# Kernel optimization log

Hardware: AMD Instinct MI355X
Metric: run time of the kernel (lower is better)

Reference implementation:

```python
import jax, jax.numpy as jnp
import numpy as np

NC = 6          # tessellation cells
THETA_D = 5     # null-space dim with zero boundary
NSTEPS = 100    # Euler integration steps for CPAB ODE
LN_EPS = 1e-5


def _cpab_basis():
    # per-cell affine params [a_i, b_i], i=0..5, vector len 12
    L = np.zeros((NC - 1 + 2, 2 * NC), dtype=np.float64)
    r = 0
    for j in range(1, NC):  # continuity at interior knots x_j = j/NC
        xj = j / NC
        L[r, 2 * (j - 1)] = xj; L[r, 2 * (j - 1) + 1] = 1.0
        L[r, 2 * j] = -xj;      L[r, 2 * j + 1] = -1.0
        r += 1
    L[r, 1] = 1.0; r += 1                                  # v(0)=0 -> b_0 = 0
    L[r, 2 * (NC - 1)] = 1.0; L[r, 2 * (NC - 1) + 1] = 1.0  # v(1)=0 -> a_5 + b_5 = 0
    _, S, Vt = np.linalg.svd(L)
    B = Vt[len(S):].T  # [12, 5] orthonormal null-space basis
    return jnp.asarray(B, dtype=jnp.float32)

B_BASIS = _cpab_basis()


def cpab_transform_grid(grid, theta):
    # grid [t] in [0,1]; theta [N, 5] -> transformed grid [N, t]
    N = theta.shape[0]
    A = (theta @ B_BASIS.T).reshape(N, NC, 2)  # [N, 6, 2] per-cell (a, b)
    x = jnp.broadcast_to(grid[None, :], (N, grid.shape[0]))
    h = 1.0 / NSTEPS

    def step(xc, _):
        idx = jnp.clip((xc * NC).astype(jnp.int32), 0, NC - 1)
        a = jnp.take_along_axis(A[:, :, 0], idx, axis=1)
        b = jnp.take_along_axis(A[:, :, 1], idx, axis=1)
        xn = jnp.clip(xc + h * (a * xc + b), 0.0, 1.0)
        return xn, None

    x, _ = jax.lax.scan(step, x, None, length=NSTEPS)
    return x


def interpolate1d(data, grid):
    # data [N, c, t]; grid [N, t_out] in [0,1] -> [N, c, t_out]
    t = data.shape[-1]
    pos = grid * (t - 1)
    x0 = jnp.clip(jnp.floor(pos).astype(jnp.int32), 0, t - 2)
    w = (pos - x0.astype(pos.dtype))[:, None, :]
    i0 = jnp.broadcast_to(x0[:, None, :], (data.shape[0], data.shape[1], grid.shape[1]))
    d0 = jnp.take_along_axis(data, i0, axis=2)
    d1 = jnp.take_along_axis(data, i0 + 1, axis=2)
    return d0 * (1.0 - w) + d1 * w


def transform_data(data, theta, t_out):
    grid = jnp.linspace(0.0, 1.0, t_out, dtype=data.dtype)
    return interpolate1d(data, cpab_transform_grid(grid, theta))


def images_to_pixels(x):
    # x [t,b,c,h,w] -> [b*h*w, c, t]
    t, b, c, h, w = x.shape
    return jnp.transpose(x, (1, 3, 4, 2, 0)).reshape(-1, c, t)


def layer_norm(x, w, b):
    m = x.mean(-1, keepdims=True)
    v = ((x - m) ** 2).mean(-1, keepdims=True)
    return (x - m) * jax.lax.rsqrt(v + LN_EPS) * w + b


def localise(x, ln_in_w, ln_in_b, conv1_w, conv1_b, conv2_w, conv2_b, ln_conv_w, ln_conv_b):
    # x [t,b,c,h,w] -> per-pixel features [b*h*w, F, t]
    t, b, c, h, w = x.shape
    z = jnp.transpose(x.reshape(t * b, c, h, w), (0, 2, 3, 1))  # [tb,h,w,c]
    z = layer_norm(z, ln_in_w, ln_in_b)
    z = jax.nn.relu(jnp.einsum('nhwc,cf->nhwf', z, conv1_w) + conv1_b)  # 1x1 conv
    z = jax.nn.relu(jnp.einsum('nhwf,fg->nhwg', z, conv2_w) + conv2_b)  # 1x1 conv
    z = layer_norm(z, ln_conv_w, ln_conv_b)
    F = z.shape[-1]
    z = z.reshape(t, b, h, w, F)
    return jnp.transpose(z, (1, 2, 3, 4, 0)).reshape(-1, F, t)


def setup_inputs() -> dict:
    key = jax.random.key(0)
    ks = jax.random.split(key, 6)
    t, b, c, h, w, F = 52, 4, 9, 64, 64, 64
    N = b * h * w
    din = 2 * F * t  # 6656
    return {
        'x': jax.random.normal(ks[0], (t, b, c, h, w), jnp.float32),
        'theta_shift_raw': jax.random.normal(ks[1], (N, THETA_D), jnp.float32),
        'ln_in_w': jnp.ones((c,), jnp.float32),
        'ln_in_b': jnp.zeros((c,), jnp.float32),
        'conv1_w': jax.random.normal(ks[2], (c, F), jnp.float32) / np.sqrt(c),
        'conv1_b': jnp.zeros((F,), jnp.float32),
        'conv2_w': jax.random.normal(ks[3], (F, F), jnp.float32) / np.sqrt(F),
        'conv2_b': jnp.zeros((F,), jnp.float32),
        'ln_conv_w': jnp.ones((F,), jnp.float32),
        'ln_conv_b': jnp.zeros((F,), jnp.float32),
        'fc1_w': jax.random.normal(ks[4], (din, 16), jnp.float32) / np.sqrt(din),
        'fc1_b': jnp.zeros((16,), jnp.float32),
        'fc2_w': jax.random.normal(ks[5], (16, THETA_D), jnp.float32) * 0.01,
        'fc2_b': jnp.zeros((THETA_D,), jnp.float32),
    }


def reference(x, theta_shift_raw, ln_in_w, ln_in_b, conv1_w, conv1_b, conv2_w, conv2_b,
              ln_conv_w, ln_conv_b, fc1_w, fc1_b, fc2_w, fc2_b):
    t, b, c, h, w = x.shape
    theta_scale = 0.5
    theta_shift = theta_scale * theta_shift_raw  # sampled transformation

    x_pix = images_to_pixels(x)  # [N, c, t]
    x_shift_pix = transform_data(x_pix, theta_shift, t)  # [N, c, t]
    # back to image stack [t,b,c,h,w]
    x_shift_img = jnp.transpose(x_shift_pix.reshape(b, h, w, c, t), (4, 0, 3, 1, 2))

    loc_args = (ln_in_w, ln_in_b, conv1_w, conv1_b, conv2_w, conv2_b, ln_conv_w, ln_conv_b)
    x_orig_loc = localise(x, *loc_args)           # [N, F, t]
    x_shift_loc = localise(x_shift_img, *loc_args)

    x_cat = jnp.concatenate((x_orig_loc, x_shift_loc), axis=1)  # [N, 2F, t]
    x_cat = x_cat.reshape(x_cat.shape[0], -1)                    # [N, 2F*t]
    theta_pred = jnp.tanh(jax.nn.relu(x_cat @ fc1_w + fc1_b) @ fc2_w + fc2_b)

    x_aligned = transform_data(x_pix, theta_pred, t)
    return (x_aligned, x_shift_pix, theta_pred, theta_shift)
```

## Files before the change

kernel.cpp:

```cpp
#include <hip/hip_runtime.h>
#include <math.h>

#define TT   52
#define BBAT 4
#define CCH  9
#define HWP  4096
#define FF   64
#define NP   16384
#define TD   5
#define NCC  6
#define TSTRIDE 147456

#define OUT0 0
#define OUT1 (NP*CCH*TT)
#define OUT2 (2*NP*CCH*TT)
#define OUT3 (OUT2 + NP*TD)

#define WS_BF    0
#define WS_WIMG  1024
#define WS_AIMG  4096
#define WS_XPIX  69632

typedef __attribute__((ext_vector_type(8)))  short short8v;
typedef __attribute__((ext_vector_type(4)))  float f32x4;
typedef __attribute__((ext_vector_type(4)))  int   int4v;
typedef __attribute__((ext_vector_type(2)))  int   int2v;

__device__ __forceinline__ unsigned bfb(float f) {
    unsigned x = __builtin_bit_cast(unsigned, f);
    return (x + 0x7fffu + ((x >> 16) & 1u)) >> 16;
}
__device__ __forceinline__ unsigned pk2(float a, float b) {
    return bfb(a) | (bfb(b) << 16);
}
__device__ __forceinline__ unsigned cvtpk(float a, float b) {
    unsigned r;
    asm("v_cvt_pk_bf16_f32 %0, %1, %2" : "=v"(r) : "v"(a), "v"(b));
    return r;
}
__device__ __forceinline__ int nswz(int n) {
    return (((n ^ (n >> 3)) & 1) << 6) | (((n >> 1) & 3) << 4);
}

__global__ __launch_bounds__(256) void k_pre(
    const float* __restrict__ lniw, const float* __restrict__ lnib,
    const float* __restrict__ w1c,  const float* __restrict__ b1c,
    const float* __restrict__ w2c,  const float* __restrict__ fc1w,
    const float* __restrict__ x,
    float* __restrict__ Bout, int4v* __restrict__ wimg,
    int4v* __restrict__ aimg, float* __restrict__ xp, int use_xp)
{
    __shared__ float ld[468 * 33];
    int blk = blockIdx.x;
    int tid = threadIdx.x;

    if (blk == 0) {
        if (tid < 64) {
            int k = tid;
            double Acol[7], Vcol[7], Mcol[5];
#pragma unroll
            for (int r = 0; r < 7; r++) { Acol[r] = 0.0; Vcol[r] = 0.0; }
#pragma unroll
            for (int j = 0; j < 5; j++) Mcol[j] = 0.0;
            if (k < 12) {
#pragma unroll
                for (int j = 1; j < 6; j++) {
                    int r = j - 1;
                    double xj = (double)j / 6.0;
                    if (k == 2 * (j - 1))     Acol[r] = xj;
                    if (k == 2 * (j - 1) + 1) Acol[r] = 1.0;
                    if (k == 2 * j)           Acol[r] = -xj;
                    if (k == 2 * j + 1)       Acol[r] = -1.0;
                }
                if (k == 1)  Acol[5] = 1.0;
                if (k == 10) Acol[6] = 1.0;
                if (k == 11) Acol[6] = 1.0;
#pragma unroll
                for (int j = 0; j < 5; j++) Mcol[j] = (k == 7 + j) ? 1.0 : 0.0;
            }
            double tau[7];
#pragma unroll
            for (int i = 0; i < 7; i++) {
                double c = (k > i && k < 12) ? Acol[i] * Acol[i] : 0.0;
#pragma unroll
                for (int off = 1; off < 64; off <<= 1) c += __shfl_xor(c, off, 64);
                double alpha = __shfl(Acol[i], i, 64);
                double t_i, vk;
                if (c == 0.0) {
                    t_i = 0.0;
                    vk = (k == i) ? 1.0 : 0.0;
                } else {
                    double nrm  = sqrt(alpha * alpha + c);
                    double beta = (alpha >= 0.0) ? -nrm : nrm;
                    t_i = (beta - alpha) / beta;
                    double inv = 1.0 / (alpha - beta);
                    vk = (k == i) ? 1.0 : ((k > i && k < 12) ? Acol[i] * inv : 0.0);
                }
                tau[i]  = t_i;
                Vcol[i] = vk;
#pragma unroll
                for (int r = 0; r < 7; r++) {
                    if (r > i) {
                        double w = Acol[r] * vk;
#pragma unroll
                        for (int off = 1; off < 64; off <<= 1) w += __shfl_xor(w, off, 64);
                        Acol[r] -= t_i * w * vk;
                    }
                }
            }
#pragma unroll
            for (int i = 6; i >= 0; i--) {
#pragma unroll
                for (int j = 0; j < 5; j++) {
                    double w = Mcol[j] * Vcol[i];
#pragma unroll
                    for (int off = 1; off < 64; off <<= 1) w += __shfl_xor(w, off, 64);
                    Mcol[j] -= tau[i] * w * Vcol[i];
                }
            }
            if (k < 12) {
#pragma unroll
                for (int j = 0; j < 5; j++) Bout[k * 5 + j] = (float)Mcol[j];
            }
        } else if (tid < 128) {
            int lane = tid - 64;
            int pl = lane & 15, h = lane >> 4;
#pragma unroll
            for (int mt = 0; mt < 4; ++mt) {
                int f = mt * 16 + pl;
                float b0f = b1c[f];
#pragma unroll
                for (int c = 0; c < 9; ++c) b0f += lnib[c] * w1c[c * 64 + f];
                float v[8];
#pragma unroll
                for (int i = 0; i < 8; ++i) {
                    int c  = h * 8 + i;
                    int cc = c < 9 ? c : 8;
                    float lv = lniw[cc] * w1c[cc * 64 + f];
                    v[i] = (c < 9) ? lv : ((c == 9) ? b0f : 0.f);
                }
                wimg[mt * 64 + lane] = (int4v){(int)pk2(v[0],v[1]), (int)pk2(v[2],v[3]),
                                               (int)pk2(v[4],v[5]), (int)pk2(v[6],v[7])};
            }
#pragma unroll
            for (int mt2 = 0; mt2 < 4; ++mt2) {
                int g = mt2 * 16 + pl;
#pragma unroll
                for (int ks = 0; ks < 2; ++ks) {
                    float v[8];
#pragma unroll
                    for (int i = 0; i < 8; ++i) v[i] = w2c[(ks * 32 + h * 8 + i) * 64 + g];
                    wimg[(4 + mt2 * 2 + ks) * 64 + lane] =
                        (int4v){(int)pk2(v[0],v[1]), (int)pk2(v[2],v[3]),
                                (int)pk2(v[4],v[5]), (int)pk2(v[6],v[7])};
                }
            }
        }
    } else if (blk <= 64) {
        int gid  = (blk - 1) * 256 + tid;
        int lane = gid & 63;
        int tc   = gid >> 6;
        int t = tc >> 5, c = tc & 31;
        int bt = t >> 2, tt0 = (t & 3) << 4;
        int m = lane & 15, h = lane >> 4;
        float v[8];
#pragma unroll
        for (int i = 0; i < 8; ++i) {
            int k = c * 32 + h * 8 + i;
            int pos_l = k >> 6, g = k & 63;
            int tt = tt0 + pos_l;
            v[i] = (tt < 52) ? fc1w[(bt * 3328 + g * 52 + tt) * 16 + m] : 0.f;
        }
        aimg[gid] = (int4v){(int)pk2(v[0],v[1]), (int)pk2(v[2],v[3]),
                            (int)pk2(v[4],v[5]), (int)pk2(v[6],v[7])};
    } else if (use_xp) {
        int b2 = blk - 65;
        int b  = b2 >> 7, pt = b2 & 127;
        int p0 = pt * 32;
        for (int idx = tid; idx < 9 * 52 * 32; idx += 256) {
            int c  = idx / 1664;
            int r  = idx - c * 1664;
            int t  = r >> 5, pp = r & 31;
            ld[(c * 52 + t) * 33 + pp] = x[((t * BBAT + b) * CCH + c) * HWP + p0 + pp];
        }
        __syncthreads();
        int wv_ = tid >> 6, ln = tid & 63;
        for (int pn = wv_; pn < 32; pn += 4) {
            float* dst = xp + (size_t)(b * HWP + p0 + pn) * 468;
#pragma unroll
            for (int e0 = 0; e0 < 468; e0 += 64) {
                int e = e0 + ln;
                if (e < 468) dst[e] = ld[e * 33 + pn];
            }
        }
    }
}

__global__ __launch_bounds__(256) void k_cpab(
    const float* __restrict__ x, const float* __restrict__ xp, int use_xp,
    const float* __restrict__ theta, const float* __restrict__ Bf,
    float scale, float* __restrict__ out,
    float* __restrict__ outts, int do_ts)
{
    __shared__ float As[256 * 13];
    __shared__ float Bs[256 * 13];
    int tid = threadIdx.x;
    int gid = blockIdx.x * 256 + tid;
    if (gid >= NP * 13) return;
    if (do_ts && gid < NP * TD) outts[gid] = 0.5f * theta[gid];
    int n  = gid / 13;
    int i0 = gid - n * 13;

    float th[TD];
#pragma unroll
    for (int j = 0; j < TD; j++) th[j] = scale * theta[n * TD + j];

#pragma unroll
    for (int i = 0; i < NCC; i++) {
        float aa = 0.f, bb = 0.f;
#pragma unroll
        for (int j = 0; j < TD; j++) {
            aa += th[j] * Bf[(2 * i) * TD + j];
            bb += th[j] * Bf[(2 * i + 1) * TD + j];
        }
        As[tid * 13 + i] = fmaf(0.01f, aa, 1.0f);
        Bs[tid * 13 + i] = 0.01f * bb;
    }
    const float* Ab = &As[tid * 13];
    const float* Bb = &Bs[tid * 13];

    float xcs[4];
#pragma unroll
    for (int c = 0; c < 4; ++c) xcs[c] = (float)(i0 + 13 * c) / 51.0f;

    for (int s = 0; s < 100; ++s) {
#pragma unroll
        for (int c = 0; c < 4; ++c) {
            int i = (int)(xcs[c] * 6.0f);
            i = i < 5 ? i : 5;
            float A = Ab[i], B = Bb[i];
            xcs[c] = __builtin_amdgcn_fmed3f(fmaf(A, xcs[c], B), 0.0f, 1.0f);
        }
    }

#pragma unroll
    for (int c2 = 0; c2 < 4; ++c2) {
        float xc = xcs[c2];
        int   tt = i0 + 13 * c2;
        float pos = xc * 51.0f;
        int x0 = (int)floorf(pos);
        if (x0 < 0) x0 = 0;
        if (x0 > 50) x0 = 50;
        float w = pos - (float)x0;
        if (use_xp) {
            const float* row = xp + (size_t)n * (CCH * TT);
#pragma unroll
            for (int ch = 0; ch < CCH; ++ch) {
                float d0 = row[ch * TT + x0];
                float d1 = row[ch * TT + x0 + 1];
                out[n * (CCH * TT) + ch * TT + tt] = d0 * (1.0f - w) + d1 * w;
            }
        } else {
            int bb_ = n >> 12, p = n & 4095;
            int base0 = ((x0 * BBAT + bb_) * CCH) * HWP + p;
#pragma unroll
            for (int ch = 0; ch < CCH; ++ch) {
                float d0 = x[base0 + ch * HWP];
                float d1 = x[base0 + ch * HWP + TSTRIDE];
                out[n * (CCH * TT) + ch * TT + tt] = d0 * (1.0f - w) + d1 * w;
            }
        }
    }
}

__global__ __launch_bounds__(512, 2) void k_loc(
    const float* __restrict__ x,
    const float* __restrict__ xs,
    const int4v* __restrict__ wimg,
    const int4v* __restrict__ aimg,
    const float* __restrict__ b2c,
    const float* __restrict__ lncw,  const float* __restrict__ lncb,
    const float* __restrict__ fc1b,
    const float* __restrict__ fc2w,  const float* __restrict__ fc2b,
    float* __restrict__ outtheta)
{
    __shared__ int4v          zcs[2][256];
    __shared__ unsigned       zchs[2][256];
    __shared__ unsigned short y1b[8][16][64];
    __shared__ unsigned short zP[16][1024];

    int tid    = threadIdx.x;
    int lane   = tid & 63;
    int wv     = tid >> 6;
    int base16 = blockIdx.x * 16;
    int bb_    = base16 >> 12, p0 = base16 & 4095;
    int pl     = lane & 15;
    int h      = lane >> 4;

    auto ln9_load = [&](int bt_, int tt_, int px_, float* dst) {
        if (tt_ < 52) {
            if (bt_ == 0) {
                int base = ((tt_ * BBAT + bb_) * CCH) * HWP + p0 + px_;
#pragma unroll
                for (int c = 0; c < 9; ++c) dst[c] = x[base + c * HWP];
            } else {
                int base = (base16 + px_) * (CCH * TT) + tt_;
#pragma unroll
                for (int c = 0; c < 9; ++c) dst[c] = xs[base + c * TT];
            }
        }
    };
    auto ln9_store = [&](int buf_, int tt_, int px_, int q_, const float* xin_) {
        float zc[9], bias;
        if (tt_ < 52) {
            float s1 = 0.f, s2 = 0.f;
#pragma unroll
            for (int c = 0; c < 9; ++c) { s1 += xin_[c]; s2 += xin_[c] * xin_[c]; }
            float m  = s1 * (1.0f / 9.0f);
            float vv = fmaxf(s2 * (1.0f / 9.0f) - m * m, 0.f);
            float rs = rsqrtf(vv + 1e-5f);
#pragma unroll
            for (int c = 0; c < 9; ++c) zc[c] = (xin_[c] - m) * rs;
            bias = 1.0f;
        } else {
#pragma unroll
            for (int c = 0; c < 9; ++c) zc[c] = 0.f;
            bias = 0.f;
        }
        zcs[buf_][px_ * 16 + (q_ ^ (px_ & 7))] =
            (int4v){(int)cvtpk(zc[0], zc[1]), (int)cvtpk(zc[2], zc[3]),
                    (int)cvtpk(zc[4], zc[5]), (int)cvtpk(zc[6], zc[7])};
        zchs[buf_][px_ * 16 + q_] = cvtpk(zc[8], bias);
    };

    short8v w1a[4], w2a[4][2];
#pragma unroll
    for (int mt = 0; mt < 4; ++mt)
        w1a[mt] = __builtin_bit_cast(short8v, wimg[mt * 64 + lane]);
#pragma unroll
    for (int mt2 = 0; mt2 < 4; ++mt2)
#pragma unroll
        for (int ks = 0; ks < 2; ++ks)
            w2a[mt2][ks] = __builtin_bit_cast(short8v, wimg[(4 + mt2 * 2 + ks) * 64 + lane]);

    f32x4 b2v[4], lw4[4], lb4[4];
#pragma unroll
    for (int mt2 = 0; mt2 < 4; ++mt2) {
        b2v[mt2] = *(const f32x4*)(b2c  + mt2 * 16 + h * 4);
        lw4[mt2] = *(const f32x4*)(lncw + mt2 * 16 + h * 4);
        lb4[mt2] = *(const f32x4*)(lncb + mt2 * 16 + h * 4);
    }

    f32x4 dacc = (f32x4){0.f, 0.f, 0.f, 0.f};

    if (tid < 256) {
        float xcur[9];
        int px = tid & 15, q = tid >> 4;
        ln9_load(0, q, px, xcur);
        ln9_store(0, q, px, q, xcur);
    }
    __syncthreads();

    for (int t = 0; t < 8; ++t) {
        int buf = t & 1;

        float xnx[9];
        int btn = (t + 1) >> 2, tt0n = ((t + 1) & 3) << 4;
        int pxn = 0, qn = 0;
        if (tid < 256 && t < 7) {
            if (btn == 0) { pxn = tid & 15; qn = tid >> 4; }
            else          { pxn = tid >> 4; qn = tid & 15; }
            ln9_load(btn, tt0n + qn, pxn, xnx);
        }

        int sw = (pl & 7) << 3;
#pragma unroll
        for (int sub = 0; sub < 2; ++sub) {
            int px = wv * 2 + sub;
            int nswp = nswz(px);

            short8v b1f;
            if (h == 1) {
                unsigned zv = zchs[buf][px * 16 + pl];
                b1f = __builtin_bit_cast(short8v, (int4v){(int)zv, 0, 0, 0});
            } else {
                b1f = __builtin_bit_cast(short8v, zcs[buf][px * 16 + (pl ^ (px & 7))]);
            }

#pragma unroll
            for (int mt = 0; mt < 4; ++mt) {
                f32x4 c1 = __builtin_amdgcn_mfma_f32_16x16x32_bf16(
                    w1a[mt], b1f, (f32x4){0.f, 0.f, 0.f, 0.f}, 0, 0, 0);
                float v0 = fmaxf(c1[0], 0.f), v1 = fmaxf(c1[1], 0.f);
                float v2 = fmaxf(c1[2], 0.f), v3 = fmaxf(c1[3], 0.f);
                int f0 = (mt * 16 + h * 4) ^ sw;
                *(int2v*)&y1b[wv][pl][f0] = (int2v){(int)cvtpk(v0, v1), (int)cvtpk(v2, v3)};
            }

            short8v b2f0 = *(const short8v*)&y1b[wv][pl][(h * 8) ^ sw];
            short8v b2f1 = *(const short8v*)&y1b[wv][pl][(32 + h * 8) ^ sw];
            float y2[4][4];
#pragma unroll
            for (int mt2 = 0; mt2 < 4; ++mt2) {
                f32x4 c2 = b2v[mt2];
                c2 = __builtin_amdgcn_mfma_f32_16x16x32_bf16(w2a[mt2][0], b2f0, c2, 0, 0, 0);
                c2 = __builtin_amdgcn_mfma_f32_16x16x32_bf16(w2a[mt2][1], b2f1, c2, 0, 0, 0);
                y2[mt2][0] = fmaxf(c2[0], 0.f);
                y2[mt2][1] = fmaxf(c2[1], 0.f);
                y2[mt2][2] = fmaxf(c2[2], 0.f);
                y2[mt2][3] = fmaxf(c2[3], 0.f);
            }

            float s = 0.f, q = 0.f;
#pragma unroll
            for (int mt2 = 0; mt2 < 4; ++mt2)
#pragma unroll
                for (int r = 0; r < 4; ++r) { s += y2[mt2][r]; q = fmaf(y2[mt2][r], y2[mt2][r], q); }
            s += __shfl_xor(s, 16, 64); s += __shfl_xor(s, 32, 64);
            q += __shfl_xor(q, 16, 64); q += __shfl_xor(q, 32, 64);
            float m2  = s * (1.0f / 64.0f);
            float v2_ = fmaxf(q * (1.0f / 64.0f) - m2 * m2, 0.f);
            float rs2 = rsqrtf(v2_ + 1e-5f);

#pragma unroll
            for (int mt2 = 0; mt2 < 4; ++mt2)
#pragma unroll
                for (int r = 0; r < 4; ++r)
                    y2[mt2][r] = fmaf((y2[mt2][r] - m2) * rs2, lw4[mt2][r], lb4[mt2][r]);

#pragma unroll
            for (int mt2 = 0; mt2 < 4; ++mt2)
#pragma unroll
                for (int rp = 0; rp < 2; ++rp) {
                    int g0 = mt2 * 16 + h * 4 + rp * 2;
                    int k2 = pl * 128 + g0 * 2;
                    int byte = (px << 11) + ((k2 ^ (((k2 >> 7) & 7) << 4)) ^ nswp);
                    *(unsigned*)((char*)zP + byte) = cvtpk(y2[mt2][rp * 2], y2[mt2][rp * 2 + 1]);
                }
        }
        __syncthreads();

        const int4v* abase = aimg + (t * 32 + wv * 4) * 64 + lane;
        int nswr = nswz(pl);
#pragma unroll
        for (int cc = 0; cc < 4; ++cc) {
            int c = wv * 4 + cc;
            short8v afrag = __builtin_bit_cast(short8v, abase[cc * 64]);
            int k2 = c * 64 + h * 16;
            int byte = (pl << 11) + ((k2 ^ (((k2 >> 7) & 7) << 4)) ^ nswr);
            short8v bfrag = *(const short8v*)((const char*)zP + byte);
            dacc = __builtin_amdgcn_mfma_f32_16x16x32_bf16(afrag, bfrag, dacc, 0, 0, 0);
        }

        if (tid < 256 && t < 7)
            ln9_store(buf ^ 1, tt0n + qn, pxn, qn, xnx);

        __syncthreads();
    }

    float* dred = (float*)zP;
    *(f32x4*)&dred[(wv * 16 + pl) * 16 + h * 4] = dacc;
    __syncthreads();
    if (tid < 256) {
        int n4 = tid >> 4, j = tid & 15;
        float hj = 0.f;
#pragma unroll
        for (int w = 0; w < 8; ++w) hj += dred[(w * 16 + n4) * 16 + j];
        hj = fmaxf(hj + fc1b[j], 0.f);
        float th[5];
#pragma unroll
        for (int d = 0; d < 5; ++d) {
            float sd = hj * fc2w[j * 5 + d];
            sd += __shfl_xor(sd, 1, 64); sd += __shfl_xor(sd, 2, 64);
            sd += __shfl_xor(sd, 4, 64); sd += __shfl_xor(sd, 8, 64);
            th[d] = sd;
        }
        if (j < 5) outtheta[(base16 + n4) * TD + j] = tanhf(th[j] + fc2b[j]);
    }
}

extern "C" void kernel_launch(void* const* d_in, const int* in_sizes, int n_in,
                              void* d_out, int out_size, void* d_ws, size_t ws_size,
                              hipStream_t stream) {
    const float* x     = (const float*)d_in[0];
    const float* thraw = (const float*)d_in[1];
    const float* lniw  = (const float*)d_in[2];
    const float* lnib  = (const float*)d_in[3];
    const float* w1c   = (const float*)d_in[4];
    const float* b1c   = (const float*)d_in[5];
    const float* w2c   = (const float*)d_in[6];
    const float* b2c   = (const float*)d_in[7];
    const float* lncw  = (const float*)d_in[8];
    const float* lncb  = (const float*)d_in[9];
    const float* fc1w  = (const float*)d_in[10];
    const float* fc1b  = (const float*)d_in[11];
    const float* fc2w  = (const float*)d_in[12];
    const float* fc2b  = (const float*)d_in[13];
    float* out  = (float*)d_out;
    float* ws   = (float*)d_ws;
    float* Bf   = ws + WS_BF;
    int4v* wimg = (int4v*)(ws + WS_WIMG);
    int4v* aimg = (int4v*)(ws + WS_AIMG);
    float* xp   = ws + WS_XPIX;
    int use_xp  = (ws_size >= (size_t)(WS_XPIX + NP * CCH * TT) * 4) ? 1 : 0;
    int npre    = use_xp ? (65 + 512) : 65;

    hipLaunchKernelGGL(k_pre, dim3(npre), dim3(256), 0, stream,
                       lniw, lnib, w1c, b1c, w2c, fc1w, x, Bf, wimg, aimg, xp, use_xp);
    hipLaunchKernelGGL(k_cpab, dim3((NP * 13) / 256), dim3(256), 0, stream,
                       x, xp, use_xp, thraw, Bf, 0.5f, out + OUT1, out + OUT3, 1);
    hipLaunchKernelGGL(k_loc, dim3(NP / 16), dim3(512), 0, stream,
                       x, out + OUT1, wimg, aimg, b2c, lncw, lncb,
                       fc1b, fc2w, fc2b, out + OUT2);
    hipLaunchKernelGGL(k_cpab, dim3((NP * 13) / 256), dim3(256), 0, stream,
                       x, xp, use_xp, out + OUT2, Bf, 1.0f, out + OUT0, out, 0);
}
```

Before: 193.3 us.

## Replace per-step Euler loop with closed-form geometric jumps within each CPAB cell

Inside a single tessellation cell the Euler update is an affine map, so k steps can be taken at once with the geometric-series formula. The kernel works out how many steps remain before the point crosses a cell boundary, jumps there using log1p/expm1, and repeats until all 100 steps are used. This replaces the fixed 100-iteration loop with a few data-dependent iterations, which introduces divergent while-loops and transcendental calls. Results may differ slightly from the step-by-step Euler iteration because of float rounding in the closed form and in the boundary step count.

Measured after the change: 617.4 us. 3.19x slower.

```diff
diff --git a/kernel.cpp b/kernel.cpp
--- a/kernel.cpp
+++ b/kernel.cpp
@@ -223,24 +223,51 @@
             aa += th[j] * Bf[(2 * i) * TD + j];
             bb += th[j] * Bf[(2 * i + 1) * TD + j];
         }
-        As[tid * 13 + i] = fmaf(0.01f, aa, 1.0f);
+        As[tid * 13 + i] = 0.01f * aa;
         Bs[tid * 13 + i] = 0.01f * bb;
     }
     const float* Ab = &As[tid * 13];
     const float* Bb = &Bs[tid * 13];
 
     float xcs[4];
-#pragma unroll
-    for (int c = 0; c < 4; ++c) xcs[c] = (float)(i0 + 13 * c) / 51.0f;
-
-    for (int s = 0; s < 100; ++s) {
-#pragma unroll
-        for (int c = 0; c < 4; ++c) {
-            int i = (int)(xcs[c] * 6.0f);
+    for (int c = 0; c < 4; ++c) {
+        float xv = (float)(i0 + 13 * c) / 51.0f;
+        int rem = 100;
+        while (rem > 0) {
+            int i = (int)(xv * 6.0f);
             i = i < 5 ? i : 5;
-            float A = Ab[i], B = Bb[i];
-            xcs[c] = __builtin_amdgcn_fmed3f(fmaf(A, xcs[c], B), 0.0f, 1.0f);
-        }
+            float hA = Ab[i], B = Bb[i];
+            float vh = fmaf(hA, xv, B);
+            if (vh == 0.0f) break;
+            float cb = (vh > 0.0f) ? (float)(i + 1) * (1.0f / 6.0f)
+                                   : (float)i * (1.0f / 6.0f);
+            float w_ = (cb - xv) / vh;
+            int k;
+            float xn;
+            if (fabsf(hA) < 1e-12f) {
+                float kf = fminf(fmaxf(w_, 0.0f), 200.0f);
+                k = (int)ceilf(kf);
+                if (k < 1) k = 1;
+                if (k > rem) k = rem;
+                xn = fmaf((float)k, vh, xv);
+            } else {
+                float lnA = log1pf(hA);
+                float u   = w_ * hA;
+                if (u <= -1.0f) {
+                    k = rem;
+                } else {
+                    float kf = log1pf(u) / lnA;
+                    kf = fminf(fmaxf(kf, 0.0f), 200.0f);
+                    k = (int)ceilf(kf);
+                    if (k < 1) k = 1;
+                    if (k > rem) k = rem;
+                }
+                xn = fmaf(expm1f((float)k * lnA) / hA, vh, xv);
+            }
+            xv = __builtin_amdgcn_fmed3f(xn, 0.0f, 1.0f);
+            rem -= k;
+        }
+        xcs[c] = xv;
     }
 
 #pragma unroll
```
